# Performance work log

Measured on AMD Instinct MI355X. Metric: run time of the kernel, lower is better.

The kernel has to match this reference:

```python
import jax, jax.numpy as jnp
import numpy as np

KERNEL = 31
GROUPS = 8
EPS = 1e-5


def mha1d(x, Wq, Wk, Wv, rel):
    """Sliding-window multi-head attention (MutliHeadAttention1D).
    x: [b, s, in_f]; Wq/Wk/Wv: [out_f, in_f] (torch Linear layout); rel: [1, out_f, KERNEL].
    Returns (out [b, s, out_f], attn [b, s, GROUPS, KERNEL])."""
    b, s, _ = x.shape
    out_f = Wq.shape[0]
    d = out_f // GROUPS
    pad = (KERNEL - 1) // 2
    xp = jnp.pad(x, ((0, 0), (pad, pad), (0, 0)))
    q = jnp.einsum('bsf,of->bso', x, Wq)          # [b, s, out_f]
    k = jnp.einsum('bsf,of->bso', xp, Wk)         # [b, s+2*pad, out_f]
    v = jnp.einsum('bsf,of->bso', xp, Wv)
    # unfold: window index [s, KERNEL]
    idx = jnp.arange(s)[:, None] + jnp.arange(KERNEL)[None, :]
    kw = jnp.swapaxes(k[:, idx], 2, 3) + rel       # [b, s, out_f, KERNEL]
    vw = jnp.swapaxes(v[:, idx], 2, 3)             # [b, s, out_f, KERNEL]
    kw = kw.reshape(b, s, GROUPS, d, KERNEL)
    vw = vw.reshape(b, s, GROUPS, d, KERNEL)
    qh = q.reshape(b, s, GROUPS, d, 1)
    energy = jnp.sum(qh * kw, axis=-2, keepdims=True)   # [b, s, g, 1, K]
    attn = jax.nn.softmax(energy, axis=-1)               # [b, s, g, 1, K]
    out = jnp.sum(attn * vw, axis=-1).reshape(b, s, out_f)
    return out, attn[:, :, :, 0, :]


def layer_norm(x, g, b):
    mu = jnp.mean(x, axis=-1, keepdims=True)
    var = jnp.mean(jnp.square(x - mu), axis=-1, keepdims=True)
    return (x - mu) / jnp.sqrt(var + EPS) * g + b


def setup_inputs() -> dict:
    key = jax.random.key(0)
    ks = jax.random.split(key, 20)
    in_f, mc, out_f = 229, 48, 88
    d = {}
    d['spec'] = jax.random.normal(ks[0], (8, 8192, in_f), dtype=jnp.float32)
    # onset attention block (in 229 -> 48)
    d['Wq1'] = jax.random.normal(ks[1], (mc, in_f), dtype=jnp.float32) * 0.1
    d['Wk1'] = jax.random.normal(ks[2], (mc, in_f), dtype=jnp.float32) * 0.1
    d['Wv1'] = jax.random.normal(ks[3], (mc, in_f), dtype=jnp.float32) * 0.1
    d['rel1'] = jax.random.normal(ks[4], (1, mc, KERNEL), dtype=jnp.float32)
    d['ln1_g'] = jnp.ones((mc,), jnp.float32)
    d['ln1_b'] = jnp.zeros((mc,), jnp.float32)
    d['Wo'] = jax.random.normal(ks[5], (out_f, mc), dtype=jnp.float32) * 0.1
    d['bo'] = jnp.zeros((out_f,), jnp.float32)
    # frame attention block (in 48+88=136 -> 48)
    in2 = mc + out_f
    d['Wq2'] = jax.random.normal(ks[6], (mc, in2), dtype=jnp.float32) * 0.1
    d['Wk2'] = jax.random.normal(ks[7], (mc, in2), dtype=jnp.float32) * 0.1
    d['Wv2'] = jax.random.normal(ks[8], (mc, in2), dtype=jnp.float32) * 0.1
    d['rel2'] = jax.random.normal(ks[9], (1, mc, KERNEL), dtype=jnp.float32)
    d['ln2_g'] = jnp.ones((mc,), jnp.float32)
    d['ln2_b'] = jnp.zeros((mc,), jnp.float32)
    d['Wf'] = jax.random.normal(ks[10], (out_f, mc), dtype=jnp.float32) * 0.1
    d['bf'] = jnp.zeros((out_f,), jnp.float32)
    return d


def reference(spec, Wq1, Wk1, Wv1, rel1, ln1_g, ln1_b, Wo, bo,
              Wq2, Wk2, Wv2, rel2, ln2_g, ln2_b, Wf, bf):
    x, a = mha1d(spec, Wq1, Wk1, Wv1, rel1)
    x = layer_norm(x, ln1_g, ln1_b)
    onset_pred = jax.nn.sigmoid(jnp.einsum('bsm,om->bso', x, Wo) + bo)
    x = jnp.concatenate((onset_pred, x), axis=-1)
    x, _ = mha1d(x, Wq2, Wk2, Wv2, rel2)
    x = layer_norm(x, ln2_g, ln2_b)
    frame_pred = jax.nn.sigmoid(jnp.einsum('bsm,om->bso', x, Wf) + bf)
    return frame_pred, onset_pred, a
```

## Files before the change

### kernel.cpp

```cpp
#include <hip/hip_runtime.h>
#include <math.h>

namespace {

constexpr int B_   = 8;
constexpr int S_   = 8192;
constexpr int NROW = B_ * S_;
constexpr int MC   = 48;
constexpr int OF   = 88;
constexpr int KW   = 31;
constexpr int F1   = 229;
constexpr int F2   = 136;

typedef __attribute__((ext_vector_type(8))) short bf16x8;
typedef __attribute__((ext_vector_type(4))) float f32x4;

__device__ inline unsigned short f2bf(float v) {
    unsigned u = __float_as_uint(v);
    unsigned r = (u + 0x7FFFu + ((u >> 16) & 1u)) >> 16;
    return (unsigned short)r;
}
__device__ inline float bf2f(unsigned short b) {
    return __uint_as_float((unsigned)b << 16);
}
__device__ inline unsigned pack2(unsigned short a, unsigned short b) {
    return (unsigned)a | ((unsigned)b << 16);
}

__global__ void wprep_kernel(const float* __restrict__ Wq,
                             const float* __restrict__ Wk,
                             const float* __restrict__ Wv,
                             int K, int nch, unsigned short* __restrict__ out) {
    int idx = blockIdx.x * 256 + threadIdx.x;
    int kpad = nch * 32;
    int total = 144 * kpad;
    if (idx >= total) return;
    int oc = idx / kpad;
    int kg = idx - oc * kpad;
    int c  = kg >> 5, kk = kg & 31;
    float val = 0.f;
    if (kg < K) {
        const float* W = (oc < 48) ? Wq : (oc < 96 ? Wk : Wv);
        int ocl = (oc < 48) ? oc : (oc < 96 ? oc - 48 : oc - 96);
        val = W[ocl * K + kg];
    }
    unsigned short h = f2bf(val);
    unsigned short l = f2bf(val - bf2f(h));
    size_t base = (size_t)c * 16384 + (size_t)oc * 56 + kk;
    out[base]        = h;
    out[base + 8192] = l;
}

__global__ void woprep_kernel(const float* __restrict__ W,
                              unsigned short* __restrict__ out) {
    int idx = blockIdx.x * 256 + threadIdx.x;
    if (idx >= 96 * 64) return;
    int n = idx >> 6, k = idx & 63;
    float val = (n < OF && k < MC) ? W[n * MC + k] : 0.f;
    unsigned short h = f2bf(val);
    unsigned short l = f2bf(val - bf2f(h));
    out[idx]        = h;
    out[6144 + idx] = l;
}

template<int K, int NCH>
__global__ __launch_bounds__(256) void proj_mfma(
    const float* __restrict__ x,
    const unsigned short* __restrict__ wbuf,
    float* __restrict__ qo, float* __restrict__ ko, float* __restrict__ vo)
{
    __shared__ __attribute__((aligned(16))) unsigned short Ah[64 * 56];
    __shared__ __attribute__((aligned(16))) unsigned short Al[64 * 56];
    __shared__ __attribute__((aligned(16))) unsigned short Bblk[16384];

    const int tid  = threadIdx.x;
    const int row0 = blockIdx.x * 64;
    const int lane = tid & 63;
    const int wm   = tid >> 6;

    f32x4 acc[9];
    #pragma unroll
    for (int nt = 0; nt < 9; ++nt) acc[nt] = f32x4{0.f, 0.f, 0.f, 0.f};

    const int arow = wm * 16 + (lane & 15);
    const int ak   = (lane >> 4) * 8;

    for (int c = 0; c < NCH; ++c) {
        {
            const uint4* src = (const uint4*)(wbuf + (size_t)c * 16384);
            uint4* dst = (uint4*)Bblk;
            #pragma unroll
            for (int i = 0; i < 8; ++i)
                dst[tid + 256 * i] = src[tid + 256 * i];
        }
        const int kc = c * 32;
        #pragma unroll
        for (int i = 0; i < 4; ++i) {
            int idx = tid + 256 * i;
            int r   = idx >> 4;
            int k2  = (idx & 15) * 2;
            int kg  = kc + k2;
            const float* xr = x + (size_t)(row0 + r) * K;
            float v0 = (kg     < K) ? xr[kg]     : 0.f;
            float v1 = (kg + 1 < K) ? xr[kg + 1] : 0.f;
            unsigned short h0 = f2bf(v0), h1 = f2bf(v1);
            unsigned short l0 = f2bf(v0 - bf2f(h0));
            unsigned short l1 = f2bf(v1 - bf2f(h1));
            *(unsigned*)&Ah[r * 56 + k2] = pack2(h0, h1);
            *(unsigned*)&Al[r * 56 + k2] = pack2(l0, l1);
        }
        __syncthreads();

        bf16x8 ah = *(const bf16x8*)&Ah[arow * 56 + ak];
        bf16x8 al = *(const bf16x8*)&Al[arow * 56 + ak];
        #pragma unroll
        for (int nt = 0; nt < 9; ++nt) {
            int bcol = nt * 16 + (lane & 15);
            bf16x8 bh = *(const bf16x8*)&Bblk[bcol * 56 + ak];
            bf16x8 bl = *(const bf16x8*)&Bblk[8192 + bcol * 56 + ak];
            acc[nt] = __builtin_amdgcn_mfma_f32_16x16x32_bf16(ah, bh, acc[nt], 0, 0, 0);
            acc[nt] = __builtin_amdgcn_mfma_f32_16x16x32_bf16(ah, bl, acc[nt], 0, 0, 0);
            acc[nt] = __builtin_amdgcn_mfma_f32_16x16x32_bf16(al, bh, acc[nt], 0, 0, 0);
        }
        __syncthreads();
    }

    const int orow = row0 + wm * 16 + ((lane >> 4) << 2);
    const int ocol = lane & 15;
    #pragma unroll
    for (int nt = 0; nt < 9; ++nt) {
        float* dst = (nt < 3) ? qo : (nt < 6 ? ko : vo);
        int oc = (nt % 3) * 16 + ocol;
        #pragma unroll
        for (int rg = 0; rg < 4; ++rg)
            dst[(size_t)(orow + rg) * MC + oc] = acc[nt][rg];
    }
}

template<bool FIRST>
__global__ __launch_bounds__(256, 4) void attn_kernel(
    const float* __restrict__ qb,
    const float* __restrict__ kb,
    const float* __restrict__ vb,
    const float* __restrict__ rel,
    const float* __restrict__ lng,
    const float* __restrict__ lnb,
    const unsigned short* __restrict__ wop,
    const float* __restrict__ bo,
    float* __restrict__ pred,
    float* __restrict__ attn_out,
    float* __restrict__ x2)
{
    __shared__ __attribute__((aligned(16))) float ks[62 * 52];
    __shared__ __attribute__((aligned(16))) float vs[62 * 52];
    __shared__ __attribute__((aligned(16))) float relT[31 * 52];
    __shared__ __attribute__((aligned(16))) unsigned short lnbuf[2][32 * 48 + 64];
    __shared__ float bosL[96];
    __shared__ float lngs[48], lnbs[48];

    const int tid  = threadIdx.x;
    const int bb   = blockIdx.x >> 8;
    const int st0  = (blockIdx.x & 255) * 32;
    const size_t base = (size_t)bb * S_;

    for (int idx = tid; idx < 744; idx += 256) {
        int rr = idx / 12, c4 = idx - rr * 12;
        int si = st0 - 15 + rr;
        float4 kv4 = {0.f, 0.f, 0.f, 0.f}, vv4 = {0.f, 0.f, 0.f, 0.f};
        if (si >= 0 && si < S_) {
            kv4 = *(const float4*)&kb[(base + si) * MC + c4 * 4];
            vv4 = *(const float4*)&vb[(base + si) * MC + c4 * 4];
        }
        *(float4*)&ks[rr * 52 + c4 * 4] = kv4;
        *(float4*)&vs[rr * 52 + c4 * 4] = vv4;
    }
    for (int idx = tid; idx < MC * KW; idx += 256) {
        int c = idx / KW, j = idx - c * KW;
        relT[j * 52 + c] = rel[idx];
    }
    if (tid < 96) bosL[tid] = (tid < OF) ? bo[tid] : 0.f;
    if (tid >= 128 && tid < 176) {
        lngs[tid - 128] = lng[tid - 128];
        lnbs[tid - 128] = lnb[tid - 128];
    }
    __syncthreads();

    const int rl  = tid >> 3;
    const int g   = tid & 7;
    const int ch0 = g * 6;
    const size_t grow = base + st0 + rl;

    const float* qr = qb + grow * MC + ch0;
    float2 q01 = *(const float2*)(qr);
    float2 q23 = *(const float2*)(qr + 2);
    float2 q45 = *(const float2*)(qr + 4);

    float e[KW];
    #pragma unroll
    for (int j = 0; j < KW; ++j) {
        const float* rp = &relT[j * 52 + ch0];
        float2 r01 = *(const float2*)(rp);
        float2 r23 = *(const float2*)(rp + 2);
        float2 r45 = *(const float2*)(rp + 4);
        e[j] = q01.x * r01.x + q01.y * r01.y + q23.x * r23.x
             + q23.y * r23.y + q45.x * r45.x + q45.y * r45.y;
    }
    float mx = -1e30f;
    #pragma unroll
    for (int j = 0; j < KW; ++j) {
        const float* kp = &ks[(rl + j) * 52 + ch0];
        float2 k01 = *(const float2*)(kp);
        float2 k23 = *(const float2*)(kp + 2);
        float2 k45 = *(const float2*)(kp + 4);
        float s = e[j] + q01.x * k01.x + q01.y * k01.y + q23.x * k23.x
                       + q23.y * k23.y + q45.x * k45.x + q45.y * k45.y;
        e[j] = s;
        mx = fmaxf(mx, s);
    }
    float den = 0.f;
    #pragma unroll
    for (int j = 0; j < KW; ++j) { float t = __expf(e[j] - mx); e[j] = t; den += t; }
    float rden = 1.f / den;

    float o0 = 0.f, o1 = 0.f, o2 = 0.f, o3 = 0.f, o4 = 0.f, o5 = 0.f;
    #pragma unroll
    for (int j = 0; j < KW; ++j) {
        float aw = e[j] * rden;
        if constexpr (FIRST) attn_out[(grow * 8 + g) * KW + j] = aw;
        const float* vp = &vs[(rl + j) * 52 + ch0];
        float2 v01 = *(const float2*)(vp);
        float2 v23 = *(const float2*)(vp + 2);
        float2 v45 = *(const float2*)(vp + 4);
        o0 += aw * v01.x; o1 += aw * v01.y; o2 += aw * v23.x;
        o3 += aw * v23.y; o4 += aw * v45.x; o5 += aw * v45.y;
    }

    float sum = o0 + o1 + o2 + o3 + o4 + o5;
    sum += __shfl_xor(sum, 1, 8);
    sum += __shfl_xor(sum, 2, 8);
    sum += __shfl_xor(sum, 4, 8);
    float mu = sum * (1.f / 48.f);
    float d0 = o0 - mu, d1 = o1 - mu, d2 = o2 - mu, d3 = o3 - mu, d4 = o4 - mu, d5 = o5 - mu;
    float vr = d0*d0 + d1*d1 + d2*d2 + d3*d3 + d4*d4 + d5*d5;
    vr += __shfl_xor(vr, 1, 8);
    vr += __shfl_xor(vr, 2, 8);
    vr += __shfl_xor(vr, 4, 8);
    float rstd = rsqrtf(vr * (1.f / 48.f) + 1e-5f);
    float y[6];
    y[0] = d0 * rstd * lngs[ch0]     + lnbs[ch0];
    y[1] = d1 * rstd * lngs[ch0 + 1] + lnbs[ch0 + 1];
    y[2] = d2 * rstd * lngs[ch0 + 2] + lnbs[ch0 + 2];
    y[3] = d3 * rstd * lngs[ch0 + 3] + lnbs[ch0 + 3];
    y[4] = d4 * rstd * lngs[ch0 + 4] + lnbs[ch0 + 4];
    y[5] = d5 * rstd * lngs[ch0 + 5] + lnbs[ch0 + 5];

    {
        unsigned short h[6], lo[6];
        #pragma unroll
        for (int c = 0; c < 6; ++c) {
            h[c]  = f2bf(y[c]);
            lo[c] = f2bf(y[c] - bf2f(h[c]));
        }
        unsigned* ph = (unsigned*)&lnbuf[0][rl * 48 + ch0];
        unsigned* pl = (unsigned*)&lnbuf[1][rl * 48 + ch0];
        ph[0] = pack2(h[0], h[1]);  ph[1] = pack2(h[2], h[3]);  ph[2] = pack2(h[4], h[5]);
        pl[0] = pack2(lo[0], lo[1]); pl[1] = pack2(lo[2], lo[3]); pl[2] = pack2(lo[4], lo[5]);
    }
    if constexpr (FIRST) {
        float* xp = x2 + grow * F2 + OF + ch0;
        *(float2*)(xp)     = float2{y[0], y[1]};
        *(float2*)(xp + 2) = float2{y[2], y[3]};
        *(float2*)(xp + 4) = float2{y[4], y[5]};
    }
    __syncthreads();

    const int l  = tid & 63;
    const int w  = tid >> 6;
    const int m  = w & 1;
    const int ng = w >> 1;
    const int lr = l & 15;
    const int lk = (l >> 4) * 8;

    bf16x8 bh[3][2], bl[3][2];
    #pragma unroll
    for (int nt = 0; nt < 3; ++nt) {
        int ncol = (ng * 3 + nt) * 16 + lr;
        #pragma unroll
        for (int kc = 0; kc < 2; ++kc) {
            size_t boff = (size_t)ncol * 64 + kc * 32 + lk;
            bh[nt][kc] = *(const bf16x8*)&wop[boff];
            bl[nt][kc] = *(const bf16x8*)&wop[6144 + boff];
        }
    }
    const int arow = m * 16 + lr;
    bf16x8 ah0 = *(const bf16x8*)&lnbuf[0][arow * 48 + lk];
    bf16x8 al0 = *(const bf16x8*)&lnbuf[1][arow * 48 + lk];
    bf16x8 ah1 = *(const bf16x8*)&lnbuf[0][arow * 48 + 32 + lk];
    bf16x8 al1 = *(const bf16x8*)&lnbuf[1][arow * 48 + 32 + lk];

    f32x4 acc[3];
    #pragma unroll
    for (int nt = 0; nt < 3; ++nt) acc[nt] = f32x4{0.f, 0.f, 0.f, 0.f};
    #pragma unroll
    for (int nt = 0; nt < 3; ++nt) {
        acc[nt] = __builtin_amdgcn_mfma_f32_16x16x32_bf16(ah0, bh[nt][0], acc[nt], 0, 0, 0);
        acc[nt] = __builtin_amdgcn_mfma_f32_16x16x32_bf16(ah0, bl[nt][0], acc[nt], 0, 0, 0);
        acc[nt] = __builtin_amdgcn_mfma_f32_16x16x32_bf16(al0, bh[nt][0], acc[nt], 0, 0, 0);
        acc[nt] = __builtin_amdgcn_mfma_f32_16x16x32_bf16(ah1, bh[nt][1], acc[nt], 0, 0, 0);
        acc[nt] = __builtin_amdgcn_mfma_f32_16x16x32_bf16(ah1, bl[nt][1], acc[nt], 0, 0, 0);
        acc[nt] = __builtin_amdgcn_mfma_f32_16x16x32_bf16(al1, bh[nt][1], acc[nt], 0, 0, 0);
    }

    const int rowo = st0 + m * 16 + ((l >> 4) << 2);
    #pragma unroll
    for (int nt = 0; nt < 3; ++nt) {
        int col = (ng * 3 + nt) * 16 + lr;
        if (col < OF) {
            float bias = bosL[col];
            #pragma unroll
            for (int rg = 0; rg < 4; ++rg) {
                float s  = acc[nt][rg] + bias;
                float sg = 1.f / (1.f + __expf(-s));
                size_t row = base + rowo + rg;
                pred[row * OF + col] = sg;
                if constexpr (FIRST) x2[row * F2 + col] = sg;
            }
        }
    }
}

}

extern "C" void kernel_launch(void* const* d_in, const int* in_sizes, int n_in,
                              void* d_out, int out_size, void* d_ws, size_t ws_size,
                              hipStream_t stream) {
    const float* spec = (const float*)d_in[0];
    const float* Wq1  = (const float*)d_in[1];
    const float* Wk1  = (const float*)d_in[2];
    const float* Wv1  = (const float*)d_in[3];
    const float* rel1 = (const float*)d_in[4];
    const float* ln1g = (const float*)d_in[5];
    const float* ln1b = (const float*)d_in[6];
    const float* Wo   = (const float*)d_in[7];
    const float* bo   = (const float*)d_in[8];
    const float* Wq2  = (const float*)d_in[9];
    const float* Wk2  = (const float*)d_in[10];
    const float* Wv2  = (const float*)d_in[11];
    const float* rel2 = (const float*)d_in[12];
    const float* ln2g = (const float*)d_in[13];
    const float* ln2b = (const float*)d_in[14];
    const float* Wf   = (const float*)d_in[15];
    const float* bf_  = (const float*)d_in[16];

    float* outf   = (float*)d_out;
    float* frame  = outf;
    float* onset  = outf + (size_t)NROW * OF;
    float* attn_a = outf + (size_t)2 * NROW * OF;

    float* wsf = (float*)d_ws;
    float* q1 = wsf;
    float* k1 = q1 + (size_t)NROW * MC;
    float* v1 = k1 + (size_t)NROW * MC;
    float* x2 = v1 + (size_t)NROW * MC;
    unsigned short* wbuf1 = (unsigned short*)(x2 + (size_t)NROW * F2);
    unsigned short* wbuf2 = wbuf1 + (size_t)8 * 16384;
    unsigned short* woP1  = wbuf2 + (size_t)5 * 16384;
    unsigned short* woP2  = woP1 + 2 * 6144;

    wprep_kernel<<<(144 * 8 * 32 + 255) / 256, 256, 0, stream>>>(Wq1, Wk1, Wv1, F1, 8, wbuf1);
    wprep_kernel<<<(144 * 5 * 32 + 255) / 256, 256, 0, stream>>>(Wq2, Wk2, Wv2, F2, 5, wbuf2);
    woprep_kernel<<<24, 256, 0, stream>>>(Wo, woP1);
    woprep_kernel<<<24, 256, 0, stream>>>(Wf, woP2);

    proj_mfma<F1, 8><<<NROW / 64, 256, 0, stream>>>(spec, wbuf1, q1, k1, v1);
    attn_kernel<true><<<NROW / 32, 256, 0, stream>>>(q1, k1, v1, rel1, ln1g, ln1b,
                                                     woP1, bo, onset, attn_a, x2);
    proj_mfma<F2, 5><<<NROW / 64, 256, 0, stream>>>(x2, wbuf2, q1, k1, v1);
    attn_kernel<false><<<NROW / 32, 256, 0, stream>>>(q1, k1, v1, rel2, ln2g, ln2b,
                                                      woP2, bf_, frame, nullptr, nullptr);
}
```

Measured before the change: 182.9 us.

## Fuse QKV projection into attention kernel with halo recompute, drop QKV round trip

Merges the bf16x3 MFMA QKV projection into the sliding-window attention kernel. Each 512-thread block projects 96 rows (64 plus a 16-row halo on each side) into shared memory, storing K/V transposed. This removes the global write and read of q/k/v and two launches, and also remaps block order and pads x2 to stride 144. The price is recomputing the halo projection (50% extra rows), using much more LDS per block, and leaving two of the eight waves idle during the projection.

```diff
diff --git a/kernel.cpp b/kernel.cpp
--- a/kernel.cpp
+++ b/kernel.cpp
@@ -11,6 +11,7 @@
 constexpr int KW   = 31;
 constexpr int F1   = 229;
 constexpr int F2   = 136;
+constexpr int X2ST = 144;
 
 typedef __attribute__((ext_vector_type(8))) short bf16x8;
 typedef __attribute__((ext_vector_type(4))) float f32x4;
@@ -63,85 +64,10 @@
     out[6144 + idx] = l;
 }
 
-template<int K, int NCH>
-__global__ __launch_bounds__(256) void proj_mfma(
+template<int K, int XST, int NCH, bool FIRST>
+__global__ __launch_bounds__(512) void fused_kernel(
     const float* __restrict__ x,
     const unsigned short* __restrict__ wbuf,
-    float* __restrict__ qo, float* __restrict__ ko, float* __restrict__ vo)
-{
-    __shared__ __attribute__((aligned(16))) unsigned short Ah[64 * 56];
-    __shared__ __attribute__((aligned(16))) unsigned short Al[64 * 56];
-    __shared__ __attribute__((aligned(16))) unsigned short Bblk[16384];
-
-    const int tid  = threadIdx.x;
-    const int row0 = blockIdx.x * 64;
-    const int lane = tid & 63;
-    const int wm   = tid >> 6;
-
-    f32x4 acc[9];
-    #pragma unroll
-    for (int nt = 0; nt < 9; ++nt) acc[nt] = f32x4{0.f, 0.f, 0.f, 0.f};
-
-    const int arow = wm * 16 + (lane & 15);
-    const int ak   = (lane >> 4) * 8;
-
-    for (int c = 0; c < NCH; ++c) {
-        {
-            const uint4* src = (const uint4*)(wbuf + (size_t)c * 16384);
-            uint4* dst = (uint4*)Bblk;
-            #pragma unroll
-            for (int i = 0; i < 8; ++i)
-                dst[tid + 256 * i] = src[tid + 256 * i];
-        }
-        const int kc = c * 32;
-        #pragma unroll
-        for (int i = 0; i < 4; ++i) {
-            int idx = tid + 256 * i;
-            int r   = idx >> 4;
-            int k2  = (idx & 15) * 2;
-            int kg  = kc + k2;
-            const float* xr = x + (size_t)(row0 + r) * K;
-            float v0 = (kg     < K) ? xr[kg]     : 0.f;
-            float v1 = (kg + 1 < K) ? xr[kg + 1] : 0.f;
-            unsigned short h0 = f2bf(v0), h1 = f2bf(v1);
-            unsigned short l0 = f2bf(v0 - bf2f(h0));
-            unsigned short l1 = f2bf(v1 - bf2f(h1));
-            *(unsigned*)&Ah[r * 56 + k2] = pack2(h0, h1);
-            *(unsigned*)&Al[r * 56 + k2] = pack2(l0, l1);
-        }
-        __syncthreads();
-
-        bf16x8 ah = *(const bf16x8*)&Ah[arow * 56 + ak];
-        bf16x8 al = *(const bf16x8*)&Al[arow * 56 + ak];
-        #pragma unroll
-        for (int nt = 0; nt < 9; ++nt) {
-            int bcol = nt * 16 + (lane & 15);
-            bf16x8 bh = *(const bf16x8*)&Bblk[bcol * 56 + ak];
-            bf16x8 bl = *(const bf16x8*)&Bblk[8192 + bcol * 56 + ak];
-            acc[nt] = __builtin_amdgcn_mfma_f32_16x16x32_bf16(ah, bh, acc[nt], 0, 0, 0);
-            acc[nt] = __builtin_amdgcn_mfma_f32_16x16x32_bf16(ah, bl, acc[nt], 0, 0, 0);
-            acc[nt] = __builtin_amdgcn_mfma_f32_16x16x32_bf16(al, bh, acc[nt], 0, 0, 0);
-        }
-        __syncthreads();
-    }
-
-    const int orow = row0 + wm * 16 + ((lane >> 4) << 2);
-    const int ocol = lane & 15;
-    #pragma unroll
-    for (int nt = 0; nt < 9; ++nt) {
-        float* dst = (nt < 3) ? qo : (nt < 6 ? ko : vo);
-        int oc = (nt % 3) * 16 + ocol;
-        #pragma unroll
-        for (int rg = 0; rg < 4; ++rg)
-            dst[(size_t)(orow + rg) * MC + oc] = acc[nt][rg];
-    }
-}
-
-template<bool FIRST>
-__global__ __launch_bounds__(256, 4) void attn_kernel(
-    const float* __restrict__ qb,
-    const float* __restrict__ kb,
-    const float* __restrict__ vb,
     const float* __restrict__ rel,
     const float* __restrict__ lng,
     const float* __restrict__ lnb,
@@ -151,30 +77,23 @@
     float* __restrict__ attn_out,
     float* __restrict__ x2)
 {
-    __shared__ __attribute__((aligned(16))) float ks[62 * 52];
-    __shared__ __attribute__((aligned(16))) float vs[62 * 52];
+    __shared__ __attribute__((aligned(16))) unsigned short Ah[96 * 40];
+    __shared__ __attribute__((aligned(16))) unsigned short Al[96 * 40];
+    __shared__ __attribute__((aligned(16))) unsigned short Bblk[16384];
+    __shared__ __attribute__((aligned(16))) float kvT[2 * 48 * 102];
+    __shared__ __attribute__((aligned(16))) float qs[64 * 52];
     __shared__ __attribute__((aligned(16))) float relT[31 * 52];
-    __shared__ __attribute__((aligned(16))) unsigned short lnbuf[2][32 * 48 + 64];
+    __shared__ __attribute__((aligned(16))) unsigned short lnbuf[2][64 * 48 + 64];
     __shared__ float bosL[96];
     __shared__ float lngs[48], lnbs[48];
 
     const int tid  = threadIdx.x;
-    const int bb   = blockIdx.x >> 8;
-    const int st0  = (blockIdx.x & 255) * 32;
+    const int bid  = ((blockIdx.x & 7) << 7) + (blockIdx.x >> 3);
+    const int bb   = bid >> 7;
+    const int st0  = (bid & 127) * 64;
     const size_t base = (size_t)bb * S_;
 
-    for (int idx = tid; idx < 744; idx += 256) {
-        int rr = idx / 12, c4 = idx - rr * 12;
-        int si = st0 - 15 + rr;
-        float4 kv4 = {0.f, 0.f, 0.f, 0.f}, vv4 = {0.f, 0.f, 0.f, 0.f};
-        if (si >= 0 && si < S_) {
-            kv4 = *(const float4*)&kb[(base + si) * MC + c4 * 4];
-            vv4 = *(const float4*)&vb[(base + si) * MC + c4 * 4];
-        }
-        *(float4*)&ks[rr * 52 + c4 * 4] = kv4;
-        *(float4*)&vs[rr * 52 + c4 * 4] = vv4;
-    }
-    for (int idx = tid; idx < MC * KW; idx += 256) {
+    for (int idx = tid; idx < MC * KW; idx += 512) {
         int c = idx / KW, j = idx - c * KW;
         relT[j * 52 + c] = rel[idx];
     }
@@ -183,6 +102,79 @@
         lngs[tid - 128] = lng[tid - 128];
         lnbs[tid - 128] = lnb[tid - 128];
     }
+    if (tid >= 192 && tid < 256) {
+        lnbuf[0][64 * 48 + tid - 192] = 0;
+        lnbuf[1][64 * 48 + tid - 192] = 0;
+    }
+
+    const int l   = tid & 63;
+    const int w   = tid >> 6;
+    const int lr  = l & 15;
+    const int lk8 = (l >> 4) * 8;
+
+    f32x4 acc[9];
+    #pragma unroll
+    for (int nt = 0; nt < 9; ++nt) acc[nt] = f32x4{0.f, 0.f, 0.f, 0.f};
+
+    for (int c = 0; c < NCH; ++c) {
+        if (c) __syncthreads();
+        {
+            const uint4* src = (const uint4*)(wbuf + (size_t)c * 16384);
+            uint4* dst = (uint4*)Bblk;
+            #pragma unroll
+            for (int i = 0; i < 4; ++i) dst[tid + 512 * i] = src[tid + 512 * i];
+        }
+        #pragma unroll
+        for (int i = 0; i < 3; ++i) {
+            int idx = tid + 512 * i;
+            int r   = idx >> 4;
+            int k2  = (idx & 15) * 2;
+            int inrow = st0 - 16 + r;
+            int kg  = c * 32 + k2;
+            bool rok = (unsigned)inrow < (unsigned)S_;
+            float v0 = (rok && kg     < K) ? x[(base + inrow) * (size_t)XST + kg]     : 0.f;
+            float v1 = (rok && kg + 1 < K) ? x[(base + inrow) * (size_t)XST + kg + 1] : 0.f;
+            unsigned short h0 = f2bf(v0), h1 = f2bf(v1);
+            unsigned short l0 = f2bf(v0 - bf2f(h0));
+            unsigned short l1 = f2bf(v1 - bf2f(h1));
+            *(unsigned*)&Ah[r * 40 + k2] = pack2(h0, h1);
+            *(unsigned*)&Al[r * 40 + k2] = pack2(l0, l1);
+        }
+        __syncthreads();
+        if (w < 6) {
+            bf16x8 ah = *(const bf16x8*)&Ah[(16 * w + lr) * 40 + lk8];
+            bf16x8 al = *(const bf16x8*)&Al[(16 * w + lr) * 40 + lk8];
+            #pragma unroll
+            for (int nt = 0; nt < 9; ++nt) {
+                int bcol = nt * 16 + lr;
+                bf16x8 bh = *(const bf16x8*)&Bblk[bcol * 56 + lk8];
+                bf16x8 bl = *(const bf16x8*)&Bblk[8192 + bcol * 56 + lk8];
+                acc[nt] = __builtin_amdgcn_mfma_f32_16x16x32_bf16(ah, bh, acc[nt], 0, 0, 0);
+                acc[nt] = __builtin_amdgcn_mfma_f32_16x16x32_bf16(ah, bl, acc[nt], 0, 0, 0);
+                acc[nt] = __builtin_amdgcn_mfma_f32_16x16x32_bf16(al, bh, acc[nt], 0, 0, 0);
+            }
+        }
+    }
+    if (w < 6) {
+        const int hb = 16 * w + ((l >> 4) << 2);
+        #pragma unroll
+        for (int nt = 3; nt < 9; ++nt) {
+            float* dT = (nt < 6) ? kvT : (kvT + 48 * 102);
+            int col = (nt - (nt < 6 ? 3 : 6)) * 16 + lr;
+            #pragma unroll
+            for (int rg = 0; rg < 4; ++rg)
+                dT[col * 102 + hb + rg] = acc[nt][rg];
+        }
+        if (w >= 1 && w <= 4) {
+            #pragma unroll
+            for (int nt = 0; nt < 3; ++nt) {
+                int col = nt * 16 + lr;
+                #pragma unroll
+                for (int rg = 0; rg < 4; ++rg)
+                    qs[(hb - 16 + rg) * 52 + col] = acc[nt][rg];
+            }
+        }
+    }
     __syncthreads();
 
     const int rl  = tid >> 3;
@@ -190,30 +182,27 @@
     const int ch0 = g * 6;
     const size_t grow = base + st0 + rl;
 
-    const float* qr = qb + grow * MC + ch0;
-    float2 q01 = *(const float2*)(qr);
-    float2 q23 = *(const float2*)(qr + 2);
-    float2 q45 = *(const float2*)(qr + 4);
+    float2 q01 = *(const float2*)&qs[rl * 52 + ch0];
+    float2 q23 = *(const float2*)&qs[rl * 52 + ch0 + 2];
+    float2 q45 = *(const float2*)&qs[rl * 52 + ch0 + 4];
+
+    const float* kT = kvT + rl + 1;
+    const float* vT = kvT + 48 * 102 + rl + 1;
 
     float e[KW];
+    float mx = -1e30f;
     #pragma unroll
     for (int j = 0; j < KW; ++j) {
         const float* rp = &relT[j * 52 + ch0];
-        float2 r01 = *(const float2*)(rp);
+        float2 r01 = *(const float2*)rp;
         float2 r23 = *(const float2*)(rp + 2);
         float2 r45 = *(const float2*)(rp + 4);
-        e[j] = q01.x * r01.x + q01.y * r01.y + q23.x * r23.x
-             + q23.y * r23.y + q45.x * r45.x + q45.y * r45.y;
-    }
-    float mx = -1e30f;
-    #pragma unroll
-    for (int j = 0; j < KW; ++j) {
-        const float* kp = &ks[(rl + j) * 52 + ch0];
-        float2 k01 = *(const float2*)(kp);
-        float2 k23 = *(const float2*)(kp + 2);
-        float2 k45 = *(const float2*)(kp + 4);
-        float s = e[j] + q01.x * k01.x + q01.y * k01.y + q23.x * k23.x
-                       + q23.y * k23.y + q45.x * k45.x + q45.y * k45.y;
+        float s = q01.x * (kT[(ch0 + 0) * 102 + j] + r01.x)
+                + q01.y * (kT[(ch0 + 1) * 102 + j] + r01.y)
+                + q23.x * (kT[(ch0 + 2) * 102 + j] + r23.x)
+                + q23.y * (kT[(ch0 + 3) * 102 + j] + r23.y)
+                + q45.x * (kT[(ch0 + 4) * 102 + j] + r45.x)
+                + q45.y * (kT[(ch0 + 5) * 102 + j] + r45.y);
         e[j] = s;
         mx = fmaxf(mx, s);
     }
@@ -227,12 +216,12 @@
     for (int j = 0; j < KW; ++j) {
         float aw = e[j] * rden;
         if constexpr (FIRST) attn_out[(grow * 8 + g) * KW + j] = aw;
-        const float* vp = &vs[(rl + j) * 52 + ch0];
-        float2 v01 = *(const float2*)(vp);
-        float2 v23 = *(const float2*)(vp + 2);
-        float2 v45 = *(const float2*)(vp + 4);
-        o0 += aw * v01.x; o1 += aw * v01.y; o2 += aw * v23.x;
-        o3 += aw * v23.y; o4 += aw * v45.x; o5 += aw * v45.y;
+        o0 += aw * vT[(ch0 + 0) * 102 + j];
+        o1 += aw * vT[(ch0 + 1) * 102 + j];
+        o2 += aw * vT[(ch0 + 2) * 102 + j];
+        o3 += aw * vT[(ch0 + 3) * 102 + j];
+        o4 += aw * vT[(ch0 + 4) * 102 + j];
+        o5 += aw * vT[(ch0 + 5) * 102 + j];
     }
 
     float sum = o0 + o1 + o2 + o3 + o4 + o5;
@@ -263,23 +252,19 @@
         }
         unsigned* ph = (unsigned*)&lnbuf[0][rl * 48 + ch0];
         unsigned* pl = (unsigned*)&lnbuf[1][rl * 48 + ch0];
-        ph[0] = pack2(h[0], h[1]);  ph[1] = pack2(h[2], h[3]);  ph[2] = pack2(h[4], h[5]);
+        ph[0] = pack2(h[0], h[1]);   ph[1] = pack2(h[2], h[3]);   ph[2] = pack2(h[4], h[5]);
         pl[0] = pack2(lo[0], lo[1]); pl[1] = pack2(lo[2], lo[3]); pl[2] = pack2(lo[4], lo[5]);
     }
     if constexpr (FIRST) {
-        float* xp = x2 + grow * F2 + OF + ch0;
+        float* xp = x2 + grow * X2ST + OF + ch0;
         *(float2*)(xp)     = float2{y[0], y[1]};
         *(float2*)(xp + 2) = float2{y[2], y[3]};
         *(float2*)(xp + 4) = float2{y[4], y[5]};
     }
     __syncthreads();
 
-    const int l  = tid & 63;
-    const int w  = tid >> 6;
-    const int m  = w & 1;
-    const int ng = w >> 1;
-    const int lr = l & 15;
-    const int lk = (l >> 4) * 8;
+    const int m  = w & 3;
+    const int ng = w >> 2;
 
     bf16x8 bh[3][2], bl[3][2];
     #pragma unroll
@@ -287,28 +272,28 @@
         int ncol = (ng * 3 + nt) * 16 + lr;
         #pragma unroll
         for (int kc = 0; kc < 2; ++kc) {
-            size_t boff = (size_t)ncol * 64 + kc * 32 + lk;
+            size_t boff = (size_t)ncol * 64 + kc * 32 + lk8;
             bh[nt][kc] = *(const bf16x8*)&wop[boff];
             bl[nt][kc] = *(const bf16x8*)&wop[6144 + boff];
         }
     }
     const int arow = m * 16 + lr;
-    bf16x8 ah0 = *(const bf16x8*)&lnbuf[0][arow * 48 + lk];
-    bf16x8 al0 = *(const bf16x8*)&lnbuf[1][arow * 48 + lk];
-    bf16x8 ah1 = *(const bf16x8*)&lnbuf[0][arow * 48 + 32 + lk];
-    bf16x8 al1 = *(const bf16x8*)&lnbuf[1][arow * 48 + 32 + lk];
-
-    f32x4 acc[3];
-    #pragma unroll
-    for (int nt = 0; nt < 3; ++nt) acc[nt] = f32x4{0.f, 0.f, 0.f, 0.f};
+    bf16x8 ah0 = *(const bf16x8*)&lnbuf[0][arow * 48 + lk8];
+    bf16x8 al0 = *(const bf16x8*)&lnbuf[1][arow * 48 + lk8];
+    bf16x8 ah1 = *(const bf16x8*)&lnbuf[0][arow * 48 + 32 + lk8];
+    bf16x8 al1 = *(const bf16x8*)&lnbuf[1][arow * 48 + 32 + lk8];
+
+    f32x4 oacc[3];
+    #pragma unroll
+    for (int nt = 0; nt < 3; ++nt) oacc[nt] = f32x4{0.f, 0.f, 0.f, 0.f};
     #pragma unroll
     for (int nt = 0; nt < 3; ++nt) {
-        acc[nt] = __builtin_amdgcn_mfma_f32_16x16x32_bf16(ah0, bh[nt][0], acc[nt], 0, 0, 0);
-        acc[nt] = __builtin_amdgcn_mfma_f32_16x16x32_bf16(ah0, bl[nt][0], acc[nt], 0, 0, 0);
-        acc[nt] = __builtin_amdgcn_mfma_f32_16x16x32_bf16(al0, bh[nt][0], acc[nt], 0, 0, 0);
-        acc[nt] = __builtin_amdgcn_mfma_f32_16x16x32_bf16(ah1, bh[nt][1], acc[nt], 0, 0, 0);
-        acc[nt] = __builtin_amdgcn_mfma_f32_16x16x32_bf16(ah1, bl[nt][1], acc[nt], 0, 0, 0);
-        acc[nt] = __builtin_amdgcn_mfma_f32_16x16x32_bf16(al1, bh[nt][1], acc[nt], 0, 0, 0);
+        oacc[nt] = __builtin_amdgcn_mfma_f32_16x16x32_bf16(ah0, bh[nt][0], oacc[nt], 0, 0, 0);
+        oacc[nt] = __builtin_amdgcn_mfma_f32_16x16x32_bf16(ah0, bl[nt][0], oacc[nt], 0, 0, 0);
+        oacc[nt] = __builtin_amdgcn_mfma_f32_16x16x32_bf16(al0, bh[nt][0], oacc[nt], 0, 0, 0);
+        oacc[nt] = __builtin_amdgcn_mfma_f32_16x16x32_bf16(ah1, bh[nt][1], oacc[nt], 0, 0, 0);
+        oacc[nt] = __builtin_amdgcn_mfma_f32_16x16x32_bf16(ah1, bl[nt][1], oacc[nt], 0, 0, 0);
+        oacc[nt] = __builtin_amdgcn_mfma_f32_16x16x32_bf16(al1, bh[nt][1], oacc[nt], 0, 0, 0);
     }
 
     const int rowo = st0 + m * 16 + ((l >> 4) << 2);
@@ -319,11 +304,11 @@
             float bias = bosL[col];
             #pragma unroll
             for (int rg = 0; rg < 4; ++rg) {
-                float s  = acc[nt][rg] + bias;
+                float s  = oacc[nt][rg] + bias;
                 float sg = 1.f / (1.f + __expf(-s));
                 size_t row = base + rowo + rg;
                 pred[row * OF + col] = sg;
-                if constexpr (FIRST) x2[row * F2 + col] = sg;
+                if constexpr (FIRST) x2[row * X2ST + col] = sg;
             }
         }
     }
@@ -358,11 +343,8 @@
     float* attn_a = outf + (size_t)2 * NROW * OF;
 
     float* wsf = (float*)d_ws;
-    float* q1 = wsf;
-    float* k1 = q1 + (size_t)NROW * MC;
-    float* v1 = k1 + (size_t)NROW * MC;
-    float* x2 = v1 + (size_t)NROW * MC;
-    unsigned short* wbuf1 = (unsigned short*)(x2 + (size_t)NROW * F2);
+    float* x2 = wsf;
+    unsigned short* wbuf1 = (unsigned short*)(x2 + (size_t)NROW * X2ST);
     unsigned short* wbuf2 = wbuf1 + (size_t)8 * 16384;
     unsigned short* woP1  = wbuf2 + (size_t)5 * 16384;
     unsigned short* woP2  = woP1 + 2 * 6144;
@@ -372,10 +354,8 @@
     woprep_kernel<<<24, 256, 0, stream>>>(Wo, woP1);
     woprep_kernel<<<24, 256, 0, stream>>>(Wf, woP2);
 
-    proj_mfma<F1, 8><<<NROW / 64, 256, 0, stream>>>(spec, wbuf1, q1, k1, v1);
-    attn_kernel<true><<<NROW / 32, 256, 0, stream>>>(q1, k1, v1, rel1, ln1g, ln1b,
-                                                     woP1, bo, onset, attn_a, x2);
-    proj_mfma<F2, 5><<<NROW / 64, 256, 0, stream>>>(x2, wbuf2, q1, k1, v1);
-    attn_kernel<false><<<NROW / 32, 256, 0, stream>>>(q1, k1, v1, rel2, ln2g, ln2b,
-                                                      woP2, bf_, frame, nullptr, nullptr);
-}
+    fused_kernel<F1, F1, 8, true><<<NROW / 64, 512, 0, stream>>>(
+        spec, wbuf1, rel1, ln1g, ln1b, woP1, bo, onset, attn_a, x2);
+    fused_kernel<F2, X2ST, 5, false><<<NROW / 64, 512, 0, stream>>>(
+        x2, wbuf2, rel2, ln2g, ln2b, woP2, bf_, frame, nullptr, nullptr);
+}
```

After: 222.5 us. 1.22x slower.

## Process two adjacent rows per thread in attention kernel with 64-row tiles

Applied to the files above, without the earlier changes.

The attention kernel now handles 64 sequence rows per block, with each thread computing two adjacent rows. The K/V and relative-position values loaded from shared memory are reused across both rows' sliding windows. The layer-norm bf16 staging buffer is aliased onto the K tile after an extra barrier, and the output projection loops over six column tiles per wave instead of holding all weight fragments. The goal is fewer LDS reads per output and less halo overhead, at the cost of more registers (two 31-entry score arrays), a dropped occupancy hint, and half as many blocks.

```diff
diff --git a/kernel.cpp b/kernel.cpp
--- a/kernel.cpp
+++ b/kernel.cpp
@@ -138,7 +138,7 @@
 }
 
 template<bool FIRST>
-__global__ __launch_bounds__(256, 4) void attn_kernel(
+__global__ __launch_bounds__(256) void attn_kernel(
     const float* __restrict__ qb,
     const float* __restrict__ kb,
     const float* __restrict__ vb,
@@ -151,19 +151,20 @@
     float* __restrict__ attn_out,
     float* __restrict__ x2)
 {
-    __shared__ __attribute__((aligned(16))) float ks[62 * 52];
-    __shared__ __attribute__((aligned(16))) float vs[62 * 52];
+    __shared__ __attribute__((aligned(16))) float ks[94 * 52];
+    __shared__ __attribute__((aligned(16))) float vs[94 * 52];
     __shared__ __attribute__((aligned(16))) float relT[31 * 52];
-    __shared__ __attribute__((aligned(16))) unsigned short lnbuf[2][32 * 48 + 64];
     __shared__ float bosL[96];
     __shared__ float lngs[48], lnbs[48];
+    unsigned short* lnh = (unsigned short*)ks;
+    unsigned short* lnl = lnh + (64 * 48 + 64);
 
     const int tid  = threadIdx.x;
-    const int bb   = blockIdx.x >> 8;
-    const int st0  = (blockIdx.x & 255) * 32;
+    const int bb   = blockIdx.x >> 7;
+    const int st0  = (blockIdx.x & 127) * 64;
     const size_t base = (size_t)bb * S_;
 
-    for (int idx = tid; idx < 744; idx += 256) {
+    for (int idx = tid; idx < 94 * 12; idx += 256) {
         int rr = idx / 12, c4 = idx - rr * 12;
         int si = st0 - 15 + rr;
         float4 kv4 = {0.f, 0.f, 0.f, 0.f}, vv4 = {0.f, 0.f, 0.f, 0.f};
@@ -185,145 +186,177 @@
     }
     __syncthreads();
 
-    const int rl  = tid >> 3;
+    const int rp  = tid >> 3;
     const int g   = tid & 7;
     const int ch0 = g * 6;
-    const size_t grow = base + st0 + rl;
-
-    const float* qr = qb + grow * MC + ch0;
-    float2 q01 = *(const float2*)(qr);
-    float2 q23 = *(const float2*)(qr + 2);
-    float2 q45 = *(const float2*)(qr + 4);
-
-    float e[KW];
+    const int rA  = 2 * rp;
+
+    const float* qpA = qb + (base + st0 + rA) * MC + ch0;
+    const float* qpB = qpA + MC;
+    float2 qa0 = *(const float2*)(qpA);
+    float2 qa1 = *(const float2*)(qpA + 2);
+    float2 qa2 = *(const float2*)(qpA + 4);
+    float2 qb0 = *(const float2*)(qpB);
+    float2 qb1 = *(const float2*)(qpB + 2);
+    float2 qb2 = *(const float2*)(qpB + 4);
+
+    float eA[KW], eB[KW];
+    float mxA = -1e30f, mxB = -1e30f;
+    float2 rp0, rp1, rp2;
+    #pragma unroll
+    for (int t = 0; t < 32; ++t) {
+        const float* kp = &ks[(rA + t) * 52 + ch0];
+        float2 k0 = *(const float2*)(kp);
+        float2 k1 = *(const float2*)(kp + 2);
+        float2 k2 = *(const float2*)(kp + 4);
+        if (t < 31) {
+            const float* rr = &relT[t * 52 + ch0];
+            float2 r0 = *(const float2*)(rr);
+            float2 r1 = *(const float2*)(rr + 2);
+            float2 r2 = *(const float2*)(rr + 4);
+            float sA = qa0.x * (k0.x + r0.x) + qa0.y * (k0.y + r0.y)
+                     + qa1.x * (k1.x + r1.x) + qa1.y * (k1.y + r1.y)
+                     + qa2.x * (k2.x + r2.x) + qa2.y * (k2.y + r2.y);
+            eA[t] = sA;
+            mxA = fmaxf(mxA, sA);
+            if (t >= 1) {
+                float sB = qb0.x * (k0.x + rp0.x) + qb0.y * (k0.y + rp0.y)
+                         + qb1.x * (k1.x + rp1.x) + qb1.y * (k1.y + rp1.y)
+                         + qb2.x * (k2.x + rp2.x) + qb2.y * (k2.y + rp2.y);
+                eB[t - 1] = sB;
+                mxB = fmaxf(mxB, sB);
+            }
+            rp0 = r0; rp1 = r1; rp2 = r2;
+        } else {
+            float sB = qb0.x * (k0.x + rp0.x) + qb0.y * (k0.y + rp0.y)
+                     + qb1.x * (k1.x + rp1.x) + qb1.y * (k1.y + rp1.y)
+                     + qb2.x * (k2.x + rp2.x) + qb2.y * (k2.y + rp2.y);
+            eB[30] = sB;
+            mxB = fmaxf(mxB, sB);
+        }
+    }
+    float denA = 0.f, denB = 0.f;
     #pragma unroll
     for (int j = 0; j < KW; ++j) {
-        const float* rp = &relT[j * 52 + ch0];
-        float2 r01 = *(const float2*)(rp);
-        float2 r23 = *(const float2*)(rp + 2);
-        float2 r45 = *(const float2*)(rp + 4);
-        e[j] = q01.x * r01.x + q01.y * r01.y + q23.x * r23.x
-             + q23.y * r23.y + q45.x * r45.x + q45.y * r45.y;
-    }
-    float mx = -1e30f;
-    #pragma unroll
-    for (int j = 0; j < KW; ++j) {
-        const float* kp = &ks[(rl + j) * 52 + ch0];
-        float2 k01 = *(const float2*)(kp);
-        float2 k23 = *(const float2*)(kp + 2);
-        float2 k45 = *(const float2*)(kp + 4);
-        float s = e[j] + q01.x * k01.x + q01.y * k01.y + q23.x * k23.x
-                       + q23.y * k23.y + q45.x * k45.x + q45.y * k45.y;
-        e[j] = s;
-        mx = fmaxf(mx, s);
-    }
-    float den = 0.f;
-    #pragma unroll
-    for (int j = 0; j < KW; ++j) { float t = __expf(e[j] - mx); e[j] = t; den += t; }
-    float rden = 1.f / den;
-
-    float o0 = 0.f, o1 = 0.f, o2 = 0.f, o3 = 0.f, o4 = 0.f, o5 = 0.f;
-    #pragma unroll
-    for (int j = 0; j < KW; ++j) {
-        float aw = e[j] * rden;
-        if constexpr (FIRST) attn_out[(grow * 8 + g) * KW + j] = aw;
-        const float* vp = &vs[(rl + j) * 52 + ch0];
-        float2 v01 = *(const float2*)(vp);
-        float2 v23 = *(const float2*)(vp + 2);
-        float2 v45 = *(const float2*)(vp + 4);
-        o0 += aw * v01.x; o1 += aw * v01.y; o2 += aw * v23.x;
-        o3 += aw * v23.y; o4 += aw * v45.x; o5 += aw * v45.y;
-    }
-
-    float sum = o0 + o1 + o2 + o3 + o4 + o5;
-    sum += __shfl_xor(sum, 1, 8);
-    sum += __shfl_xor(sum, 2, 8);
-    sum += __shfl_xor(sum, 4, 8);
-    float mu = sum * (1.f / 48.f);
-    float d0 = o0 - mu, d1 = o1 - mu, d2 = o2 - mu, d3 = o3 - mu, d4 = o4 - mu, d5 = o5 - mu;
-    float vr = d0*d0 + d1*d1 + d2*d2 + d3*d3 + d4*d4 + d5*d5;
-    vr += __shfl_xor(vr, 1, 8);
-    vr += __shfl_xor(vr, 2, 8);
-    vr += __shfl_xor(vr, 4, 8);
-    float rstd = rsqrtf(vr * (1.f / 48.f) + 1e-5f);
-    float y[6];
-    y[0] = d0 * rstd * lngs[ch0]     + lnbs[ch0];
-    y[1] = d1 * rstd * lngs[ch0 + 1] + lnbs[ch0 + 1];
-    y[2] = d2 * rstd * lngs[ch0 + 2] + lnbs[ch0 + 2];
-    y[3] = d3 * rstd * lngs[ch0 + 3] + lnbs[ch0 + 3];
-    y[4] = d4 * rstd * lngs[ch0 + 4] + lnbs[ch0 + 4];
-    y[5] = d5 * rstd * lngs[ch0 + 5] + lnbs[ch0 + 5];
+        float tA = __expf(eA[j] - mxA); eA[j] = tA; denA += tA;
+        float tB = __expf(eB[j] - mxB); eB[j] = tB; denB += tB;
+    }
+    const float rdA = 1.f / denA, rdB = 1.f / denB;
+
+    float oA0=0.f,oA1=0.f,oA2=0.f,oA3=0.f,oA4=0.f,oA5=0.f;
+    float oB0=0.f,oB1=0.f,oB2=0.f,oB3=0.f,oB4=0.f,oB5=0.f;
+    float* aoutA = FIRST ? (attn_out + ((base + st0 + rA) * 8 + g) * KW) : nullptr;
+    #pragma unroll
+    for (int t = 0; t < 32; ++t) {
+        const float* vp = &vs[(rA + t) * 52 + ch0];
+        float2 v0 = *(const float2*)(vp);
+        float2 v1 = *(const float2*)(vp + 2);
+        float2 v2 = *(const float2*)(vp + 4);
+        if (t < 31) {
+            float aw = eA[t] * rdA;
+            if constexpr (FIRST) aoutA[t] = aw;
+            oA0 += aw * v0.x; oA1 += aw * v0.y; oA2 += aw * v1.x;
+            oA3 += aw * v1.y; oA4 += aw * v2.x; oA5 += aw * v2.y;
+        }
+        if (t >= 1) {
+            float aw = eB[t - 1] * rdB;
+            if constexpr (FIRST) aoutA[8 * KW + t - 1] = aw;
+            oB0 += aw * v0.x; oB1 += aw * v0.y; oB2 += aw * v1.x;
+            oB3 += aw * v1.y; oB4 += aw * v2.x; oB5 += aw * v2.y;
+        }
+    }
+
+    float sA = oA0+oA1+oA2+oA3+oA4+oA5;
+    float sB = oB0+oB1+oB2+oB3+oB4+oB5;
+    sA += __shfl_xor(sA, 1, 8); sA += __shfl_xor(sA, 2, 8); sA += __shfl_xor(sA, 4, 8);
+    sB += __shfl_xor(sB, 1, 8); sB += __shfl_xor(sB, 2, 8); sB += __shfl_xor(sB, 4, 8);
+    float muA = sA * (1.f / 48.f), muB = sB * (1.f / 48.f);
+    float dA0=oA0-muA,dA1=oA1-muA,dA2=oA2-muA,dA3=oA3-muA,dA4=oA4-muA,dA5=oA5-muA;
+    float dB0=oB0-muB,dB1=oB1-muB,dB2=oB2-muB,dB3=oB3-muB,dB4=oB4-muB,dB5=oB5-muB;
+    float vA = dA0*dA0+dA1*dA1+dA2*dA2+dA3*dA3+dA4*dA4+dA5*dA5;
+    float vB = dB0*dB0+dB1*dB1+dB2*dB2+dB3*dB3+dB4*dB4+dB5*dB5;
+    vA += __shfl_xor(vA, 1, 8); vA += __shfl_xor(vA, 2, 8); vA += __shfl_xor(vA, 4, 8);
+    vB += __shfl_xor(vB, 1, 8); vB += __shfl_xor(vB, 2, 8); vB += __shfl_xor(vB, 4, 8);
+    float rsA = rsqrtf(vA * (1.f / 48.f) + 1e-5f);
+    float rsB = rsqrtf(vB * (1.f / 48.f) + 1e-5f);
+    float yA[6], yB[6];
+    yA[0]=dA0*rsA*lngs[ch0]+lnbs[ch0];     yA[1]=dA1*rsA*lngs[ch0+1]+lnbs[ch0+1];
+    yA[2]=dA2*rsA*lngs[ch0+2]+lnbs[ch0+2]; yA[3]=dA3*rsA*lngs[ch0+3]+lnbs[ch0+3];
+    yA[4]=dA4*rsA*lngs[ch0+4]+lnbs[ch0+4]; yA[5]=dA5*rsA*lngs[ch0+5]+lnbs[ch0+5];
+    yB[0]=dB0*rsB*lngs[ch0]+lnbs[ch0];     yB[1]=dB1*rsB*lngs[ch0+1]+lnbs[ch0+1];
+    yB[2]=dB2*rsB*lngs[ch0+2]+lnbs[ch0+2]; yB[3]=dB3*rsB*lngs[ch0+3]+lnbs[ch0+3];
+    yB[4]=dB4*rsB*lngs[ch0+4]+lnbs[ch0+4]; yB[5]=dB5*rsB*lngs[ch0+5]+lnbs[ch0+5];
+
+    if constexpr (FIRST) {
+        float* xpA = x2 + (base + st0 + rA) * F2 + OF + ch0;
+        *(float2*)(xpA)     = float2{yA[0], yA[1]};
+        *(float2*)(xpA + 2) = float2{yA[2], yA[3]};
+        *(float2*)(xpA + 4) = float2{yA[4], yA[5]};
+        float* xpB = xpA + F2;
+        *(float2*)(xpB)     = float2{yB[0], yB[1]};
+        *(float2*)(xpB + 2) = float2{yB[2], yB[3]};
+        *(float2*)(xpB + 4) = float2{yB[4], yB[5]};
+    }
+
+    __syncthreads();
 
     {
-        unsigned short h[6], lo[6];
+        unsigned short hA[6], lA[6], hB[6], lB[6];
         #pragma unroll
         for (int c = 0; c < 6; ++c) {
-            h[c]  = f2bf(y[c]);
-            lo[c] = f2bf(y[c] - bf2f(h[c]));
-        }
-        unsigned* ph = (unsigned*)&lnbuf[0][rl * 48 + ch0];
-        unsigned* pl = (unsigned*)&lnbuf[1][rl * 48 + ch0];
-        ph[0] = pack2(h[0], h[1]);  ph[1] = pack2(h[2], h[3]);  ph[2] = pack2(h[4], h[5]);
-        pl[0] = pack2(lo[0], lo[1]); pl[1] = pack2(lo[2], lo[3]); pl[2] = pack2(lo[4], lo[5]);
-    }
-    if constexpr (FIRST) {
-        float* xp = x2 + grow * F2 + OF + ch0;
-        *(float2*)(xp)     = float2{y[0], y[1]};
-        *(float2*)(xp + 2) = float2{y[2], y[3]};
-        *(float2*)(xp + 4) = float2{y[4], y[5]};
+            hA[c] = f2bf(yA[c]); lA[c] = f2bf(yA[c] - bf2f(hA[c]));
+            hB[c] = f2bf(yB[c]); lB[c] = f2bf(yB[c] - bf2f(hB[c]));
+        }
+        unsigned* pha = (unsigned*)&lnh[rA * 48 + ch0];
+        unsigned* pla = (unsigned*)&lnl[rA * 48 + ch0];
+        pha[0] = pack2(hA[0], hA[1]); pha[1] = pack2(hA[2], hA[3]); pha[2] = pack2(hA[4], hA[5]);
+        pla[0] = pack2(lA[0], lA[1]); pla[1] = pack2(lA[2], lA[3]); pla[2] = pack2(lA[4], lA[5]);
+        unsigned* phb = (unsigned*)&lnh[(rA + 1) * 48 + ch0];
+        unsigned* plb = (unsigned*)&lnl[(rA + 1) * 48 + ch0];
+        phb[0] = pack2(hB[0], hB[1]); phb[1] = pack2(hB[2], hB[3]); phb[2] = pack2(hB[4], hB[5]);
+        plb[0] = pack2(lB[0], lB[1]); plb[1] = pack2(lB[2], lB[3]); plb[2] = pack2(lB[4], lB[5]);
+    }
+    if (tid < 64) {
+        lnh[64 * 48 + tid] = 0;
+        lnl[64 * 48 + tid] = 0;
     }
     __syncthreads();
 
-    const int l  = tid & 63;
-    const int w  = tid >> 6;
-    const int m  = w & 1;
-    const int ng = w >> 1;
-    const int lr = l & 15;
-    const int lk = (l >> 4) * 8;
-
-    bf16x8 bh[3][2], bl[3][2];
-    #pragma unroll
-    for (int nt = 0; nt < 3; ++nt) {
-        int ncol = (ng * 3 + nt) * 16 + lr;
-        #pragma unroll
-        for (int kc = 0; kc < 2; ++kc) {
-            size_t boff = (size_t)ncol * 64 + kc * 32 + lk;
-            bh[nt][kc] = *(const bf16x8*)&wop[boff];
-            bl[nt][kc] = *(const bf16x8*)&wop[6144 + boff];
-        }
-    }
-    const int arow = m * 16 + lr;
-    bf16x8 ah0 = *(const bf16x8*)&lnbuf[0][arow * 48 + lk];
-    bf16x8 al0 = *(const bf16x8*)&lnbuf[1][arow * 48 + lk];
-    bf16x8 ah1 = *(const bf16x8*)&lnbuf[0][arow * 48 + 32 + lk];
-    bf16x8 al1 = *(const bf16x8*)&lnbuf[1][arow * 48 + 32 + lk];
-
-    f32x4 acc[3];
-    #pragma unroll
-    for (int nt = 0; nt < 3; ++nt) acc[nt] = f32x4{0.f, 0.f, 0.f, 0.f};
-    #pragma unroll
-    for (int nt = 0; nt < 3; ++nt) {
-        acc[nt] = __builtin_amdgcn_mfma_f32_16x16x32_bf16(ah0, bh[nt][0], acc[nt], 0, 0, 0);
-        acc[nt] = __builtin_amdgcn_mfma_f32_16x16x32_bf16(ah0, bl[nt][0], acc[nt], 0, 0, 0);
-        acc[nt] = __builtin_amdgcn_mfma_f32_16x16x32_bf16(al0, bh[nt][0], acc[nt], 0, 0, 0);
-        acc[nt] = __builtin_amdgcn_mfma_f32_16x16x32_bf16(ah1, bh[nt][1], acc[nt], 0, 0, 0);
-        acc[nt] = __builtin_amdgcn_mfma_f32_16x16x32_bf16(ah1, bl[nt][1], acc[nt], 0, 0, 0);
-        acc[nt] = __builtin_amdgcn_mfma_f32_16x16x32_bf16(al1, bh[nt][1], acc[nt], 0, 0, 0);
-    }
-
-    const int rowo = st0 + m * 16 + ((l >> 4) << 2);
-    #pragma unroll
-    for (int nt = 0; nt < 3; ++nt) {
-        int col = (ng * 3 + nt) * 16 + lr;
-        if (col < OF) {
-            float bias = bosL[col];
+    const int l   = tid & 63;
+    const int w   = tid >> 6;
+    const int lr  = l & 15;
+    const int lk8 = (l >> 4) * 8;
+
+    const int arow = w * 16 + lr;
+    bf16x8 ah0 = *(const bf16x8*)&lnh[arow * 48 + lk8];
+    bf16x8 al0 = *(const bf16x8*)&lnl[arow * 48 + lk8];
+    bf16x8 ah1 = *(const bf16x8*)&lnh[arow * 48 + 32 + lk8];
+    bf16x8 al1 = *(const bf16x8*)&lnl[arow * 48 + 32 + lk8];
+
+    const int rowo = st0 + w * 16 + ((l >> 4) << 2);
+    #pragma unroll
+    for (int nt = 0; nt < 6; ++nt) {
+        int ncol = nt * 16 + lr;
+        bf16x8 bh0 = *(const bf16x8*)&wop[(size_t)ncol * 64 + lk8];
+        bf16x8 bl0 = *(const bf16x8*)&wop[6144 + (size_t)ncol * 64 + lk8];
+        bf16x8 bh1 = *(const bf16x8*)&wop[(size_t)ncol * 64 + 32 + lk8];
+        bf16x8 bl1 = *(const bf16x8*)&wop[6144 + (size_t)ncol * 64 + 32 + lk8];
+        f32x4 oacc = f32x4{0.f, 0.f, 0.f, 0.f};
+        oacc = __builtin_amdgcn_mfma_f32_16x16x32_bf16(ah0, bh0, oacc, 0, 0, 0);
+        oacc = __builtin_amdgcn_mfma_f32_16x16x32_bf16(ah0, bl0, oacc, 0, 0, 0);
+        oacc = __builtin_amdgcn_mfma_f32_16x16x32_bf16(al0, bh0, oacc, 0, 0, 0);
+        oacc = __builtin_amdgcn_mfma_f32_16x16x32_bf16(ah1, bh1, oacc, 0, 0, 0);
+        oacc = __builtin_amdgcn_mfma_f32_16x16x32_bf16(ah1, bl1, oacc, 0, 0, 0);
+        oacc = __builtin_amdgcn_mfma_f32_16x16x32_bf16(al1, bh1, oacc, 0, 0, 0);
+        if (ncol < OF) {
+            float bias = bosL[ncol];
             #pragma unroll
             for (int rg = 0; rg < 4; ++rg) {
-                float s  = acc[nt][rg] + bias;
+                float s  = oacc[rg] + bias;
                 float sg = 1.f / (1.f + __expf(-s));
                 size_t row = base + rowo + rg;
-                pred[row * OF + col] = sg;
-                if constexpr (FIRST) x2[row * F2 + col] = sg;
+                pred[row * OF + ncol] = sg;
+                if constexpr (FIRST) x2[row * F2 + ncol] = sg;
             }
         }
     }
@@ -373,9 +406,9 @@
     woprep_kernel<<<24, 256, 0, stream>>>(Wf, woP2);
 
     proj_mfma<F1, 8><<<NROW / 64, 256, 0, stream>>>(spec, wbuf1, q1, k1, v1);
-    attn_kernel<true><<<NROW / 32, 256, 0, stream>>>(q1, k1, v1, rel1, ln1g, ln1b,
+    attn_kernel<true><<<NROW / 64, 256, 0, stream>>>(q1, k1, v1, rel1, ln1g, ln1b,
                                                      woP1, bo, onset, attn_a, x2);
     proj_mfma<F2, 5><<<NROW / 64, 256, 0, stream>>>(x2, wbuf2, q1, k1, v1);
-    attn_kernel<false><<<NROW / 32, 256, 0, stream>>>(q1, k1, v1, rel2, ln2g, ln2b,
+    attn_kernel<false><<<NROW / 64, 256, 0, stream>>>(q1, k1, v1, rel2, ln2g, ln2b,
                                                       woP2, bf_, frame, nullptr, nullptr);
 }
```

Result: no change. 184.3 us (+0.8%).
